# Performance work log

Hardware: AMD Instinct MI355X
Metric: run time of the kernel (lower is better)

Reference implementation:

```python
import jax, jax.numpy as jnp
import numpy as np

N_NODES = 50000
N_EDGES = 800000
IN_NODE = 256
IN_EDGE = 64
OUT_DIM = 128


def setup_inputs() -> dict:
    key = jax.random.key(0)
    k1, k2, k3, k4, k5, k6, k7 = jax.random.split(key, 7)
    feats_node = jax.random.normal(k1, (N_NODES, IN_NODE), dtype=jnp.float32)
    feats_edge = jax.random.normal(k2, (N_EDGES, IN_EDGE), dtype=jnp.float32)
    src = jax.random.randint(k3, (N_EDGES,), 0, N_NODES, dtype=jnp.int32)
    dst = jax.random.randint(k4, (N_EDGES,), 0, N_NODES, dtype=jnp.int32)
    # weights init: normal(std=0.5), torch Linear stores [out, in]
    Wn = 0.5 * jax.random.normal(k5, (OUT_DIM, IN_NODE), dtype=jnp.float32)
    We = 0.5 * jax.random.normal(k6, (IN_EDGE, IN_EDGE), dtype=jnp.float32)
    Wa = 0.5 * jax.random.normal(k7, (1, 2 * OUT_DIM + IN_EDGE), dtype=jnp.float32)
    return {"feats_node": feats_node, "feats_edge": feats_edge,
            "src": src, "dst": dst, "Wn": Wn, "We": We, "Wa": Wa}


def reference(feats_node, feats_edge, src, dst, Wn, We, Wa):
    n_nodes = feats_node.shape[0]
    # node / edge projections
    z = feats_node @ Wn.T            # [N, out_dim]
    ze = feats_edge @ We.T           # [E, in_dim_edge]
    # per-edge attention logit: attn_fc(cat(z_src, z_dst, z_edge)) + leaky_relu
    z3 = jnp.concatenate([z[src], z[dst], ze], axis=1)   # [E, 2*out+edge]
    a = z3 @ Wa.T                                        # [E, 1]
    e = jax.nn.leaky_relu(a, negative_slope=0.2)[:, 0]   # [E]
    # segment softmax over incoming edges of each dst node (numerically stable)
    m = jax.ops.segment_max(e, dst, num_segments=n_nodes)        # [N]
    m = jnp.where(jnp.isfinite(m), m, 0.0)                       # isolated nodes
    e_exp = jnp.exp(e - m[dst])                                  # [E]
    denom = jax.ops.segment_sum(e_exp, dst, num_segments=n_nodes)  # [N]
    alpha = e_exp / jnp.maximum(denom[dst], 1e-38)               # [E]
    # weighted scatter-sum of source messages
    h = jax.ops.segment_sum(alpha[:, None] * z[src], dst, num_segments=n_nodes)
    return h, ze
```

## Files before the change

kernel.cpp:

```cpp
#include <hip/hip_runtime.h>
#include <hip/hip_bf16.h>
#include <math.h>

#define N_NODES 50000
#define N_EDGES 800000
#define IN_NODE 256
#define IN_EDGE 64
#define OUT_DIM 128

typedef __attribute__((ext_vector_type(8))) short short8;
typedef __attribute__((ext_vector_type(4))) float f32x4;

__device__ inline short f2bf(float x) {
    union { float f; unsigned u; } v; v.f = x;
    unsigned r = v.u + 0x7fff + ((v.u >> 16) & 1);
    return (short)(r >> 16);
}

__device__ inline void cvt_store8(short* p, float4 a, float4 b) {
    union { short h[8]; uint4 u; } t;
    t.h[0] = f2bf(a.x); t.h[1] = f2bf(a.y); t.h[2] = f2bf(a.z); t.h[3] = f2bf(a.w);
    t.h[4] = f2bf(b.x); t.h[5] = f2bf(b.y); t.h[6] = f2bf(b.z); t.h[7] = f2bf(b.w);
    *(uint4*)p = t.u;
}

__global__ __launch_bounds__(256) void k0_prep(
    const float* __restrict__ We, const float* __restrict__ Wn,
    const float* __restrict__ Wa,
    float* __restrict__ v_e, float* __restrict__ u_src, float* __restrict__ u_dst)
{
    const int k = threadIdx.x;
    if (k < IN_EDGE) {
        float s = 0.f;
        for (int c = 0; c < IN_EDGE; ++c)
            s += We[c * IN_EDGE + k] * Wa[2 * OUT_DIM + c];
        v_e[k] = s;
    }
    float a = 0.f, b = 0.f;
    for (int c = 0; c < OUT_DIM; ++c) {
        const float w = Wn[(size_t)c * IN_NODE + k];
        a += Wa[c] * w;
        b += Wa[OUT_DIM + c] * w;
    }
    u_src[k] = a;
    u_dst[k] = b;
}

__global__ __launch_bounds__(256) void k_deg(const int* __restrict__ dst,
                                             int* __restrict__ deg)
{
    const int i = (blockIdx.x * 256 + threadIdx.x) * 4;
    if (i < N_EDGES) {
        const int4 d = *(const int4*)&dst[i];
        atomicAdd(&deg[d.x], 1);
        atomicAdd(&deg[d.y], 1);
        atomicAdd(&deg[d.z], 1);
        atomicAdd(&deg[d.w], 1);
    }
}

#define K1_BK 64

__global__ __launch_bounds__(256) void k1_node_mfma(
    const float* __restrict__ fn, const float* __restrict__ Wn,
    const float* __restrict__ u_src, const float* __restrict__ u_dst,
    __hip_bfloat16* __restrict__ zb,
    float* __restrict__ s_src, float* __restrict__ s_dst)
{
    __shared__ alignas(16) short A_lds[128][72];
    __shared__ alignas(16) short B_lds[128][72];

    const int t    = threadIdx.x;
    const int lane = t & 63;
    const int w    = t >> 6;
    const int m0   = blockIdx.x * 128;

    const int nd   = t >> 1;
    const int half = t & 1;

    int grow = m0 + nd; if (grow >= N_NODES) grow = N_NODES - 1;
    const float* arow = &fn[(size_t)grow * IN_NODE];
    const float* brow = &Wn[(size_t)nd * IN_NODE];

    float sa = 0.f, sb = 0.f;

    const int lrow = lane & 15;
    const int lk   = (lane >> 4) * 8;

    f32x4 acc[2][8];
    for (int r = 0; r < 2; ++r)
        for (int c = 0; c < 8; ++c)
            acc[r][c] = (f32x4){0.f, 0.f, 0.f, 0.f};

    for (int k0 = 0; k0 < IN_NODE; k0 += K1_BK) {
        {
            const float4* rp = (const float4*)&arow[k0 + half * 32];
            float4 va[8];
            for (int q = 0; q < 8; ++q) va[q] = rp[q];
            for (int q = 0; q < 8; ++q) {
                const float4 us = *(const float4*)&u_src[k0 + half * 32 + q * 4];
                const float4 ud = *(const float4*)&u_dst[k0 + half * 32 + q * 4];
                sa += va[q].x * us.x + va[q].y * us.y + va[q].z * us.z + va[q].w * us.w;
                sb += va[q].x * ud.x + va[q].y * ud.y + va[q].z * ud.z + va[q].w * ud.w;
            }
            short* wp = &A_lds[nd][half * 32];
            for (int q = 0; q < 4; ++q)
                cvt_store8(wp + q * 8, va[2 * q], va[2 * q + 1]);
        }
        {
            const float4* rp = (const float4*)&brow[k0 + half * 32];
            float4 vb[8];
            for (int q = 0; q < 8; ++q) vb[q] = rp[q];
            short* wp = &B_lds[nd][half * 32];
            for (int q = 0; q < 4; ++q)
                cvt_store8(wp + q * 8, vb[2 * q], vb[2 * q + 1]);
        }
        __syncthreads();

        for (int s = 0; s < 2; ++s) {
            const int kk = s * 32 + lk;
            short8 aF[2], bF[8];
            for (int r = 0; r < 2; ++r)
                aF[r] = *(const short8*)&A_lds[w * 32 + r * 16 + lrow][kk];
            for (int c = 0; c < 8; ++c)
                bF[c] = *(const short8*)&B_lds[c * 16 + lrow][kk];
            for (int r = 0; r < 2; ++r)
                for (int c = 0; c < 8; ++c)
                    acc[r][c] = __builtin_amdgcn_mfma_f32_16x16x32_bf16(
                        aF[r], bF[c], acc[r][c], 0, 0, 0);
        }
        __syncthreads();
    }

    {
        const float oa = __shfl_xor(sa, 1, 64);
        const float ob = __shfl_xor(sb, 1, 64);
        if (half == 0 && (m0 + nd) < N_NODES) {
            s_src[m0 + nd] = sa + oa;
            s_dst[m0 + nd] = sb + ob;
        }
    }

    const int rq = lane >> 4;
    for (int r = 0; r < 2; ++r) {
        for (int reg = 0; reg < 4; ++reg) {
            const int row = m0 + w * 32 + r * 16 + rq * 4 + reg;
            if (row < N_NODES) {
                for (int c = 0; c < 8; ++c)
                    zb[(size_t)row * OUT_DIM + c * 16 + lrow] =
                        __float2bfloat16(acc[r][c][reg]);
            }
        }
    }
}

__global__ __launch_bounds__(256) void k2_edge_gemm_mfma(
    const float* __restrict__ fe, const float* __restrict__ We,
    const float* __restrict__ v_e,
    const int* __restrict__ src, const int* __restrict__ dst,
    const float* __restrict__ s_src, const float* __restrict__ s_dst,
    int* __restrict__ cursor,
    float* __restrict__ ze_out, int* __restrict__ csr_src,
    float* __restrict__ csr_e)
{
    __shared__ alignas(16) short A_lds[128][72];
    __shared__ alignas(16) short B_lds[64][72];
    __shared__ float se_lds[128];

    const int t    = threadIdx.x;
    const int lane = t & 63;
    const int w    = t >> 6;
    const long e0  = (long)blockIdx.x * 128;

    {
        const int edge = t >> 1, half = t & 1;
        const float4* rp = (const float4*)&fe[(e0 + edge) * IN_EDGE + half * 32];
        float4 va[8];
        for (int q = 0; q < 8; ++q) va[q] = rp[q];

        float part = 0.f;
        for (int q = 0; q < 8; ++q) {
            const float4 w4 = *(const float4*)&v_e[half * 32 + q * 4];
            part += va[q].x * w4.x + va[q].y * w4.y
                  + va[q].z * w4.z + va[q].w * w4.w;
        }
        const float other = __shfl_xor(part, 1, 64);
        if (half == 0) se_lds[edge] = part + other;

        short* wp = &A_lds[edge][half * 32];
        for (int q = 0; q < 4; ++q)
            cvt_store8(wp + q * 8, va[2 * q], va[2 * q + 1]);
    }
    {
        const int row = t >> 2, kq = (t & 3) * 16;
        const float4* rp = (const float4*)&We[(size_t)row * IN_EDGE + kq];
        cvt_store8(&B_lds[row][kq + 0], rp[0], rp[1]);
        cvt_store8(&B_lds[row][kq + 8], rp[2], rp[3]);
    }
    __syncthreads();

    const int lrow = lane & 15;
    const int lk   = (lane >> 4) * 8;

    f32x4 acc[2][4];
    for (int r = 0; r < 2; ++r)
        for (int c = 0; c < 4; ++c)
            acc[r][c] = (f32x4){0.f, 0.f, 0.f, 0.f};

    for (int s = 0; s < 2; ++s) {
        const int kk = s * 32 + lk;
        short8 aF[2], bF[4];
        for (int r = 0; r < 2; ++r)
            aF[r] = *(const short8*)&A_lds[w * 32 + r * 16 + lrow][kk];
        for (int c = 0; c < 4; ++c)
            bF[c] = *(const short8*)&B_lds[c * 16 + lrow][kk];
        for (int r = 0; r < 2; ++r)
            for (int c = 0; c < 4; ++c)
                acc[r][c] = __builtin_amdgcn_mfma_f32_16x16x32_bf16(
                    aF[r], bF[c], acc[r][c], 0, 0, 0);
    }

    const int rquad = lane >> 4;
    for (int r = 0; r < 2; ++r) {
        for (int c = 0; c < 4; ++c) {
            for (int reg = 0; reg < 4; ++reg) {
                const long row = e0 + w * 32 + r * 16 + rquad * 4 + reg;
                ze_out[row * IN_EDGE + c * 16 + lrow] = acc[r][c][reg];
            }
        }
    }

    if (t < 128) {
        const long e = e0 + t;
        const int d = dst[e];
        const int s = src[e];
        float lg = s_src[s] + s_dst[d] + se_lds[t];
        lg = (lg > 0.f) ? lg : 0.2f * lg;
        const int pos = atomicAdd(&cursor[d], 1);
        csr_src[pos] = s;
        csr_e[pos]   = lg;
    }
}

#define SCAN_T 1024
#define SCAN_C 49

__global__ __launch_bounds__(SCAN_T) void k4_scan(
    const int* __restrict__ deg, int* __restrict__ off, int* __restrict__ cursor)
{
    __shared__ int part[SCAN_T];
    const int t = threadIdx.x;
    const int lo = t * SCAN_C;
    int hi = lo + SCAN_C; if (hi > N_NODES) hi = N_NODES;

    int s = 0;
    for (int i = lo; i < hi; ++i) s += deg[i];
    part[t] = s;
    __syncthreads();
    for (int d = 1; d < SCAN_T; d <<= 1) {
        int v = 0;
        if (t >= d) v = part[t - d];
        __syncthreads();
        if (t >= d) part[t] += v;
        __syncthreads();
    }
    int run = (t == 0) ? 0 : part[t - 1];
    for (int i = lo; i < hi; ++i) {
        off[i] = run; cursor[i] = run;
        run += deg[i];
    }
    if (t == SCAN_T - 1) off[N_NODES] = part[SCAN_T - 1];
}

__global__ __launch_bounds__(256) void k6_aggregate(
    const int* __restrict__ off, const int* __restrict__ csr_src,
    const float* __restrict__ csr_e, const __hip_bfloat16* __restrict__ zb,
    float* __restrict__ h)
{
    const int node = (int)((blockIdx.x * blockDim.x + threadIdx.x) >> 6);
    const int lane = threadIdx.x & 63;
    if (node >= N_NODES) return;

    const int beg = off[node];
    const int end = off[node + 1];
    const int deg = end - beg;

    const int cgrp = lane & 15;
    const int eidx = lane >> 4;

    float out[8] = {0.f, 0.f, 0.f, 0.f, 0.f, 0.f, 0.f, 0.f};

    if (deg > 0) {
        float m = -INFINITY;
        for (int j = lane; j < deg; j += 64) m = fmaxf(m, csr_e[beg + j]);
        for (int o = 32; o > 0; o >>= 1) m = fmaxf(m, __shfl_xor(m, o, 64));

        float l = 0.f;
        for (int c0 = 0; c0 < deg; c0 += 64) {
            const int cl = min(64, deg - c0);
            float wv = 0.f;
            if (lane < cl) wv = __expf(csr_e[beg + c0 + lane] - m);
            float ws = wv;
            for (int o = 32; o > 0; o >>= 1) ws += __shfl_xor(ws, o, 64);
            l += ws;

            for (int jj = 0; jj < cl; jj += 4) {
                const int j  = jj + eidx;
                const int jc = (j < cl) ? j : (cl - 1);
                const float wgt = __shfl(wv, jc, 64);
                if (j < cl) {
                    const int s = csr_src[beg + c0 + j];
                    const uint4 zv = *(const uint4*)&zb[(size_t)s * OUT_DIM + cgrp * 8];
                    const unsigned* zu = (const unsigned*)&zv;
                    for (int q = 0; q < 4; ++q) {
                        out[2 * q]     += wgt * __uint_as_float(zu[q] << 16);
                        out[2 * q + 1] += wgt * __uint_as_float(zu[q] & 0xffff0000u);
                    }
                }
            }
        }
        for (int i = 0; i < 8; ++i) {
            out[i] += __shfl_xor(out[i], 16, 64);
            out[i] += __shfl_xor(out[i], 32, 64);
        }
        const float inv = 1.f / fmaxf(l, 1e-38f);
        for (int i = 0; i < 8; ++i) out[i] *= inv;
    }

    if (lane < 16) {
        float4 o0 = make_float4(out[0], out[1], out[2], out[3]);
        float4 o1 = make_float4(out[4], out[5], out[6], out[7]);
        float* hp = &h[(size_t)node * OUT_DIM + lane * 8];
        *(float4*)(hp + 0) = o0;
        *(float4*)(hp + 4) = o1;
    }
}

extern "C" void kernel_launch(void* const* d_in, const int* in_sizes, int n_in,
                              void* d_out, int out_size, void* d_ws, size_t ws_size,
                              hipStream_t stream)
{
    const float* fn  = (const float*)d_in[0];
    const float* fe  = (const float*)d_in[1];
    const int*   src = (const int*)d_in[2];
    const int*   dst = (const int*)d_in[3];
    const float* Wn  = (const float*)d_in[4];
    const float* We  = (const float*)d_in[5];
    const float* Wa  = (const float*)d_in[6];

    float* h_out  = (float*)d_out;
    float* ze_out = h_out + (size_t)N_NODES * OUT_DIM;

    char* p = (char*)d_ws;
    auto alloc = [&](size_t bytes) -> char* {
        char* r = p;
        p += (bytes + 255) & ~(size_t)255;
        return r;
    };
    __hip_bfloat16* zb = (__hip_bfloat16*)alloc((size_t)N_NODES * OUT_DIM * 2);
    float* s_src   = (float*)alloc((size_t)N_NODES * 4);
    float* s_dst   = (float*)alloc((size_t)N_NODES * 4);
    int*   deg     = (int*)alloc((size_t)N_NODES * 4);
    int*   off     = (int*)alloc((size_t)(N_NODES + 1) * 4);
    int*   cursor  = (int*)alloc((size_t)N_NODES * 4);
    int*   csr_src = (int*)alloc((size_t)N_EDGES * 4);
    float* csr_e   = (float*)alloc((size_t)N_EDGES * 4);
    float* v_e     = (float*)alloc((size_t)IN_EDGE * 4);
    float* u_src   = (float*)alloc((size_t)IN_NODE * 4);
    float* u_dst   = (float*)alloc((size_t)IN_NODE * 4);

    hipMemsetAsync(deg, 0, (size_t)N_NODES * sizeof(int), stream);

    k0_prep<<<1, 256, 0, stream>>>(We, Wn, Wa, v_e, u_src, u_dst);
    k_deg<<<(N_EDGES / 4 + 255) / 256, 256, 0, stream>>>(dst, deg);
    k4_scan<<<1, SCAN_T, 0, stream>>>(deg, off, cursor);
    k1_node_mfma<<<(N_NODES + 127) / 128, 256, 0, stream>>>(
        fn, Wn, u_src, u_dst, zb, s_src, s_dst);
    k2_edge_gemm_mfma<<<N_EDGES / 128, 256, 0, stream>>>(
        fe, We, v_e, src, dst, s_src, s_dst, cursor, ze_out, csr_src, csr_e);
    k6_aggregate<<<(N_NODES + 3) / 4, 256, 0, stream>>>(
        off, csr_src, csr_e, zb, h_out);
}
```

Before: 664.4 us.

## Stage edge GEMM output through LDS for coalesced stores, merge prep kernel

Edge GEMM results are now staged through LDS, reusing the A tile buffer in two 64-row passes, and then written to ze_out as coalesced 16-byte nontemporal stores. Before, each thread wrote scattered 4-byte stores. The per-edge CSR scatter and logit computation moves ahead of the MFMA loop so its latency can overlap with the matrix work. The weight-folding prep kernel is merged into the degree-count kernel's block 0, which removes one launch. In exchange, the kernel gains extra __syncthreads barriers and one block of the degree kernel carries the serial prep work.

```diff
diff --git a/kernel.cpp b/kernel.cpp
--- a/kernel.cpp
+++ b/kernel.cpp
@@ -24,30 +24,11 @@
     *(uint4*)p = t.u;
 }
 
-__global__ __launch_bounds__(256) void k0_prep(
+__global__ __launch_bounds__(256) void k_deg_prep(
+    const int* __restrict__ dst, int* __restrict__ deg,
     const float* __restrict__ We, const float* __restrict__ Wn,
     const float* __restrict__ Wa,
     float* __restrict__ v_e, float* __restrict__ u_src, float* __restrict__ u_dst)
-{
-    const int k = threadIdx.x;
-    if (k < IN_EDGE) {
-        float s = 0.f;
-        for (int c = 0; c < IN_EDGE; ++c)
-            s += We[c * IN_EDGE + k] * Wa[2 * OUT_DIM + c];
-        v_e[k] = s;
-    }
-    float a = 0.f, b = 0.f;
-    for (int c = 0; c < OUT_DIM; ++c) {
-        const float w = Wn[(size_t)c * IN_NODE + k];
-        a += Wa[c] * w;
-        b += Wa[OUT_DIM + c] * w;
-    }
-    u_src[k] = a;
-    u_dst[k] = b;
-}
-
-__global__ __launch_bounds__(256) void k_deg(const int* __restrict__ dst,
-                                             int* __restrict__ deg)
 {
     const int i = (blockIdx.x * 256 + threadIdx.x) * 4;
     if (i < N_EDGES) {
@@ -56,6 +37,23 @@
         atomicAdd(&deg[d.y], 1);
         atomicAdd(&deg[d.z], 1);
         atomicAdd(&deg[d.w], 1);
+    }
+    if (blockIdx.x == 0) {
+        const int k = threadIdx.x;
+        if (k < IN_EDGE) {
+            float s = 0.f;
+            for (int c = 0; c < IN_EDGE; ++c)
+                s += We[c * IN_EDGE + k] * Wa[2 * OUT_DIM + c];
+            v_e[k] = s;
+        }
+        float a = 0.f, b = 0.f;
+        for (int c = 0; c < OUT_DIM; ++c) {
+            const float w = Wn[(size_t)c * IN_NODE + k];
+            a += Wa[c] * w;
+            b += Wa[OUT_DIM + c] * w;
+        }
+        u_src[k] = a;
+        u_dst[k] = b;
     }
 }
 
@@ -167,6 +165,8 @@
     __shared__ alignas(16) short B_lds[64][72];
     __shared__ float se_lds[128];
 
+    float (*zt)[68] = reinterpret_cast<float(*)[68]>(&A_lds[0][0]);
+
     const int t    = threadIdx.x;
     const int lane = t & 63;
     const int w    = t >> 6;
@@ -198,6 +198,17 @@
         cvt_store8(&B_lds[row][kq + 8], rp[2], rp[3]);
     }
     __syncthreads();
+
+    if (t < 128) {
+        const long e = e0 + t;
+        const int d = dst[e];
+        const int s = src[e];
+        float lg = s_src[s] + s_dst[d] + se_lds[t];
+        lg = (lg > 0.f) ? lg : 0.2f * lg;
+        const int pos = atomicAdd(&cursor[d], 1);
+        csr_src[pos] = s;
+        csr_e[pos]   = lg;
+    }
 
     const int lrow = lane & 15;
     const int lk   = (lane >> 4) * 8;
@@ -221,24 +232,25 @@
     }
 
     const int rquad = lane >> 4;
-    for (int r = 0; r < 2; ++r) {
-        for (int c = 0; c < 4; ++c) {
-            for (int reg = 0; reg < 4; ++reg) {
-                const long row = e0 + w * 32 + r * 16 + rquad * 4 + reg;
-                ze_out[row * IN_EDGE + c * 16 + lrow] = acc[r][c][reg];
-            }
-        }
-    }
-
-    if (t < 128) {
-        const long e = e0 + t;
-        const int d = dst[e];
-        const int s = src[e];
-        float lg = s_src[s] + s_dst[d] + se_lds[t];
-        lg = (lg > 0.f) ? lg : 0.2f * lg;
-        const int pos = atomicAdd(&cursor[d], 1);
-        csr_src[pos] = s;
-        csr_e[pos]   = lg;
+    for (int p = 0; p < 2; ++p) {
+        __syncthreads();
+        if ((w >> 1) == p) {
+            const int rb = w * 32 - p * 64;
+            for (int r = 0; r < 2; ++r)
+                for (int c = 0; c < 4; ++c)
+                    for (int reg = 0; reg < 4; ++reg)
+                        zt[rb + r * 16 + rquad * 4 + reg][c * 16 + lrow] =
+                            acc[r][c][reg];
+        }
+        __syncthreads();
+        for (int it = 0; it < 4; ++it) {
+            const int idx = it * 256 + t;
+            const int row = idx >> 4;
+            const int c4  = idx & 15;
+            const f32x4 v = *(const f32x4*)&zt[row][c4 * 4];
+            __builtin_nontemporal_store(
+                v, (f32x4*)&ze_out[(e0 + p * 64 + row) * IN_EDGE + c4 * 4]);
+        }
     }
 }
 
@@ -371,8 +383,8 @@
 
     hipMemsetAsync(deg, 0, (size_t)N_NODES * sizeof(int), stream);
 
-    k0_prep<<<1, 256, 0, stream>>>(We, Wn, Wa, v_e, u_src, u_dst);
-    k_deg<<<(N_EDGES / 4 + 255) / 256, 256, 0, stream>>>(dst, deg);
+    k_deg_prep<<<(N_EDGES / 4 + 255) / 256, 256, 0, stream>>>(
+        dst, deg, We, Wn, Wa, v_e, u_src, u_dst);
     k4_scan<<<1, SCAN_T, 0, stream>>>(deg, off, cursor);
     k1_node_mfma<<<(N_NODES + 127) / 128, 256, 0, stream>>>(
         fn, Wn, u_src, u_dst, zb, s_src, s_dst);
```

Result: faster. 648.3 us (-2.4%).
